# Optimization experiments

Measured on AMD Instinct MI355X. Metric: run time of the kernel, lower is better.

Reference implementation:

```python
import jax, jax.numpy as jnp
import numpy as np

GAMMA = 0.5
BATCH, DIM, UNITS = 16384, 512, 1024


def setup_inputs() -> dict:
    key = jax.random.key(0)
    k1, k2 = jax.random.split(key)
    inputs = jax.random.normal(k1, (BATCH, DIM), dtype=jnp.float32)
    mu = jax.random.normal(k2, (DIM, UNITS), dtype=jnp.float32)
    return {"inputs": inputs, "mu": mu}


def reference(inputs, mu):
    # Squared L2 distance from each input row to each center (column of mu):
    x_sq = jnp.sum(inputs * inputs, axis=1, keepdims=True)        # [B, 1]
    mu_sq = jnp.sum(mu * mu, axis=0, keepdims=True)               # [1, U]
    cross = inputs @ mu                                           # [B, U] GEMM
    l2 = x_sq - 2.0 * cross + mu_sq                                # [B, U]
    return jnp.exp(-GAMMA * l2)
```

## Files before the change

kernel.cpp:

```cpp
#include <hip/hip_runtime.h>
#include <hip/hip_bf16.h>

#define BATCH 16384
#define DIM   512
#define UNITS 1024

typedef float v16f __attribute__((ext_vector_type(16)));

#define APITCH 516
#define BPITCH 33

__global__ __launch_bounds__(256)
void prep_kernel(const float* __restrict__ in, const float* __restrict__ mu,
                 unsigned char* __restrict__ A8f, unsigned char* __restrict__ B8f,
                 float* __restrict__ xsq, float* __restrict__ musq) {
    __shared__ __attribute__((aligned(16))) char smem[512 * BPITCH * 4 + 1024];
    const int t  = threadIdx.x;
    const int l  = t & 63, w = t >> 6;
    const int ln = l & 31, h = l >> 5;

    if (blockIdx.x >= UNITS / 32) {
        float* lds = (float*)smem;
        float* red = (float*)(smem + 32 * APITCH * 4);
        const int c = blockIdx.x - UNITS / 32;
        const float4* src = (const float4*)(in + (size_t)c * 32 * DIM);
        float4* l4 = (float4*)lds;
#pragma unroll
        for (int i = 0; i < 16; i++) {
            const int f = i * 256 + t;
            l4[(f >> 7) * (APITCH / 4) + (f & 127)] = src[f];
        }
        __syncthreads();
        float s = 0.f;
#pragma unroll
        for (int j = 0; j < 8; j++) {
            const int kw = w * 8 + j;
            const float* p = lds + ln * APITCH + kw * 16 + h * 8;
            float4 f0 = *(const float4*)p;
            float4 f1 = *(const float4*)(p + 4);
            s += f0.x * f0.x + f0.y * f0.y + f0.z * f0.z + f0.w * f0.w
               + f1.x * f1.x + f1.y * f1.y + f1.z * f1.z + f1.w * f1.w;
            int lo = __builtin_amdgcn_cvt_pk_fp8_f32(f0.x, f0.y, 0, false);
            lo     = __builtin_amdgcn_cvt_pk_fp8_f32(f0.z, f0.w, lo, true);
            int hi = __builtin_amdgcn_cvt_pk_fp8_f32(f1.x, f1.y, 0, false);
            hi     = __builtin_amdgcn_cvt_pk_fp8_f32(f1.z, f1.w, hi, true);
            *(int2*)(A8f + (((size_t)c * 32 + kw) * 64 + l) * 8) = make_int2(lo, hi);
        }
        red[ln * 8 + w * 2 + h] = s;
        __syncthreads();
        if (t < 32) {
            float a = 0.f;
#pragma unroll
            for (int i = 0; i < 8; i++) a += red[t * 8 + i];
            xsq[c * 32 + t] = a;
        }
    } else {
        float* lds = (float*)smem;
        float* red = (float*)(smem + 512 * BPITCH * 4);
        const int nb = blockIdx.x;
        const int n0 = nb * 32;
        const int col = t & 31, kg = t >> 5;
        float s = 0.f;
        for (int i = 0; i < 64; i++) {
            const int k = i * 8 + kg;
            float v = mu[(size_t)k * UNITS + n0 + col];
            s += v * v;
            lds[k * BPITCH + col] = v;
        }
        red[col * 8 + kg] = s;
        __syncthreads();
        if (t < 32) {
            float a = 0.f;
#pragma unroll
            for (int i = 0; i < 8; i++) a += red[t * 8 + i];
            musq[n0 + t] = a;
        }
#pragma unroll
        for (int j = 0; j < 8; j++) {
            const int kw = w * 8 + j;
            const float* p = lds + (kw * 16 + h * 8) * BPITCH + ln;
            float f[8];
#pragma unroll
            for (int i = 0; i < 8; i++) f[i] = p[i * BPITCH];
            int lo = __builtin_amdgcn_cvt_pk_fp8_f32(f[0], f[1], 0, false);
            lo     = __builtin_amdgcn_cvt_pk_fp8_f32(f[2], f[3], lo, true);
            int hi = __builtin_amdgcn_cvt_pk_fp8_f32(f[4], f[5], 0, false);
            hi     = __builtin_amdgcn_cvt_pk_fp8_f32(f[6], f[7], hi, true);
            *(int2*)(B8f + (((size_t)nb * 32 + kw) * 64 + l) * 8) = make_int2(lo, hi);
        }
    }
}

__global__ __launch_bounds__(256, 4)
void rbf_gemm_kernel(const unsigned char* __restrict__ A8f,
                     const unsigned char* __restrict__ B8f,
                     const float* __restrict__ xsq,
                     const float* __restrict__ musq,
                     float* __restrict__ out) {
    const int t  = threadIdx.x;
    const int l  = t & 63;
    const int w  = t >> 6;
    const int ln = l & 31;
    const int h  = l >> 5;

    const int b  = blockIdx.x;
    const int x  = b & 7;
    const int q  = b >> 3;
    const int rg = q & 15;
    const int cg = q >> 4;
    const int m0 = x * 2048 + rg * 128 + (w >> 1) * 64;
    const int n0 = cg * 128 + (w & 1) * 64;

    const long* Af = (const long*)A8f + (size_t)(m0 >> 5) * 2048 + l;
    const long* Bf = (const long*)B8f + (size_t)(n0 >> 5) * 2048 + l;

    v16f acc[2][2];
#pragma unroll
    for (int c = 0; c < 2; c++)
#pragma unroll
        for (int j = 0; j < 2; j++) acc[c][j] = (v16f)0.f;

#pragma unroll 4
    for (int kw = 0; kw < 32; kw++) {
        long a0 = Af[kw * 64];
        long a1 = Af[2048 + kw * 64];
        long b0 = Bf[kw * 64];
        long b1 = Bf[2048 + kw * 64];
        acc[0][0] = __builtin_amdgcn_mfma_f32_32x32x16_fp8_fp8(a0, b0, acc[0][0], 0, 0, 0);
        acc[0][1] = __builtin_amdgcn_mfma_f32_32x32x16_fp8_fp8(a0, b1, acc[0][1], 0, 0, 0);
        acc[1][0] = __builtin_amdgcn_mfma_f32_32x32x16_fp8_fp8(a1, b0, acc[1][0], 0, 0, 0);
        acc[1][1] = __builtin_amdgcn_mfma_f32_32x32x16_fp8_fp8(a1, b1, acc[1][1], 0, 0, 0);
    }

#pragma unroll
    for (int c = 0; c < 2; c++) {
        const int mc = m0 + c * 32;
        const float xv = -0.5f * xsq[mc + ln];
#pragma unroll
        for (int j = 0; j < 2; j++) {
            const int nc = n0 + j * 32;
            const float mb = -0.5f * musq[nc + ln];
#pragma unroll
            for (int r = 0; r < 16; r++) {
                const int rl = (r & 3) + 8 * (r >> 2) + 4 * h;
                const float xb = __shfl(xv, rl, 64);
                float v = __expf(acc[c][j][r] + xb + mb);
                __builtin_nontemporal_store(
                    v, out + (size_t)(mc + rl) * UNITS + nc + ln);
            }
        }
    }
}

extern "C" void kernel_launch(void* const* d_in, const int* in_sizes, int n_in,
                              void* d_out, int out_size, void* d_ws, size_t ws_size,
                              hipStream_t stream) {
    const float* inputs = (const float*)d_in[0];
    const float* mu     = (const float*)d_in[1];
    float* out = (float*)d_out;

    char* ws = (char*)d_ws;
    unsigned char* A8f = (unsigned char*)ws;
    unsigned char* B8f = (unsigned char*)(ws + (size_t)BATCH * DIM);
    float* xsq  = (float*)(ws + (size_t)BATCH * DIM + (size_t)UNITS * DIM);
    float* musq = xsq + BATCH;

    prep_kernel<<<UNITS / 32 + BATCH / 32, 256, 0, stream>>>(
        inputs, mu, A8f, B8f, xsq, musq);
    rbf_gemm_kernel<<<1024, 256, 0, stream>>>(A8f, B8f, xsq, musq, out);
}
```

Before: 117.6 us.

## Fuse input FP8 quantization and row norms into the GEMM kernel

The prep kernel now only handles mu (FP8 conversion and column norms). Input rows are loaded, squared-summed and converted to FP8 directly inside the GEMM kernel, which stages each 32-row A strip in LDS. Each 512-thread block covers 32 rows by all 1024 units, with each wave computing four 32x32 tiles from a shared A fragment. This removes the write and reread of the FP8 A buffer and the xsq round trip. In exchange, B is reread from global/L2 by every block and the tile shape changes data reuse.

New measurement: 122.9 us. 1.05x slower.

```diff
diff --git a/kernel.cpp b/kernel.cpp
--- a/kernel.cpp
+++ b/kernel.cpp
@@ -7,147 +7,114 @@
 
 typedef float v16f __attribute__((ext_vector_type(16)));
 
-#define APITCH 516
 #define BPITCH 33
+#define FPITCH 520
 
 __global__ __launch_bounds__(256)
-void prep_kernel(const float* __restrict__ in, const float* __restrict__ mu,
-                 unsigned char* __restrict__ A8f, unsigned char* __restrict__ B8f,
-                 float* __restrict__ xsq, float* __restrict__ musq) {
+void prep_b_kernel(const float* __restrict__ mu, unsigned char* __restrict__ B8f,
+                   float* __restrict__ musq) {
     __shared__ __attribute__((aligned(16))) char smem[512 * BPITCH * 4 + 1024];
+    float* lds = (float*)smem;
+    float* red = (float*)(smem + 512 * BPITCH * 4);
     const int t  = threadIdx.x;
     const int l  = t & 63, w = t >> 6;
     const int ln = l & 31, h = l >> 5;
-
-    if (blockIdx.x >= UNITS / 32) {
-        float* lds = (float*)smem;
-        float* red = (float*)(smem + 32 * APITCH * 4);
-        const int c = blockIdx.x - UNITS / 32;
-        const float4* src = (const float4*)(in + (size_t)c * 32 * DIM);
-        float4* l4 = (float4*)lds;
+    const int nb = blockIdx.x;
+    const int n0 = nb * 32;
+    const int col = t & 31, kg = t >> 5;
+    float s = 0.f;
+    for (int i = 0; i < 64; i++) {
+        const int k = i * 8 + kg;
+        float v = mu[(size_t)k * UNITS + n0 + col];
+        s += v * v;
+        lds[k * BPITCH + col] = v;
+    }
+    red[col * 8 + kg] = s;
+    __syncthreads();
+    if (t < 32) {
+        float a = 0.f;
 #pragma unroll
-        for (int i = 0; i < 16; i++) {
-            const int f = i * 256 + t;
-            l4[(f >> 7) * (APITCH / 4) + (f & 127)] = src[f];
-        }
-        __syncthreads();
-        float s = 0.f;
+        for (int i = 0; i < 8; i++) a += red[t * 8 + i];
+        musq[n0 + t] = a;
+    }
 #pragma unroll
-        for (int j = 0; j < 8; j++) {
-            const int kw = w * 8 + j;
-            const float* p = lds + ln * APITCH + kw * 16 + h * 8;
-            float4 f0 = *(const float4*)p;
-            float4 f1 = *(const float4*)(p + 4);
-            s += f0.x * f0.x + f0.y * f0.y + f0.z * f0.z + f0.w * f0.w
-               + f1.x * f1.x + f1.y * f1.y + f1.z * f1.z + f1.w * f1.w;
-            int lo = __builtin_amdgcn_cvt_pk_fp8_f32(f0.x, f0.y, 0, false);
-            lo     = __builtin_amdgcn_cvt_pk_fp8_f32(f0.z, f0.w, lo, true);
-            int hi = __builtin_amdgcn_cvt_pk_fp8_f32(f1.x, f1.y, 0, false);
-            hi     = __builtin_amdgcn_cvt_pk_fp8_f32(f1.z, f1.w, hi, true);
-            *(int2*)(A8f + (((size_t)c * 32 + kw) * 64 + l) * 8) = make_int2(lo, hi);
-        }
-        red[ln * 8 + w * 2 + h] = s;
-        __syncthreads();
-        if (t < 32) {
-            float a = 0.f;
+    for (int j = 0; j < 8; j++) {
+        const int kw = w * 8 + j;
+        const float* p = lds + (kw * 16 + h * 8) * BPITCH + ln;
+        float f[8];
 #pragma unroll
-            for (int i = 0; i < 8; i++) a += red[t * 8 + i];
-            xsq[c * 32 + t] = a;
-        }
-    } else {
-        float* lds = (float*)smem;
-        float* red = (float*)(smem + 512 * BPITCH * 4);
-        const int nb = blockIdx.x;
-        const int n0 = nb * 32;
-        const int col = t & 31, kg = t >> 5;
-        float s = 0.f;
-        for (int i = 0; i < 64; i++) {
-            const int k = i * 8 + kg;
-            float v = mu[(size_t)k * UNITS + n0 + col];
-            s += v * v;
-            lds[k * BPITCH + col] = v;
-        }
-        red[col * 8 + kg] = s;
-        __syncthreads();
-        if (t < 32) {
-            float a = 0.f;
-#pragma unroll
-            for (int i = 0; i < 8; i++) a += red[t * 8 + i];
-            musq[n0 + t] = a;
-        }
-#pragma unroll
-        for (int j = 0; j < 8; j++) {
-            const int kw = w * 8 + j;
-            const float* p = lds + (kw * 16 + h * 8) * BPITCH + ln;
-            float f[8];
-#pragma unroll
-            for (int i = 0; i < 8; i++) f[i] = p[i * BPITCH];
-            int lo = __builtin_amdgcn_cvt_pk_fp8_f32(f[0], f[1], 0, false);
-            lo     = __builtin_amdgcn_cvt_pk_fp8_f32(f[2], f[3], lo, true);
-            int hi = __builtin_amdgcn_cvt_pk_fp8_f32(f[4], f[5], 0, false);
-            hi     = __builtin_amdgcn_cvt_pk_fp8_f32(f[6], f[7], hi, true);
-            *(int2*)(B8f + (((size_t)nb * 32 + kw) * 64 + l) * 8) = make_int2(lo, hi);
-        }
+        for (int i = 0; i < 8; i++) f[i] = p[i * BPITCH];
+        int lo = __builtin_amdgcn_cvt_pk_fp8_f32(f[0], f[1], 0, false);
+        lo     = __builtin_amdgcn_cvt_pk_fp8_f32(f[2], f[3], lo, true);
+        int hi = __builtin_amdgcn_cvt_pk_fp8_f32(f[4], f[5], 0, false);
+        hi     = __builtin_amdgcn_cvt_pk_fp8_f32(f[6], f[7], hi, true);
+        *(int2*)(B8f + (((size_t)nb * 32 + kw) * 64 + l) * 8) = make_int2(lo, hi);
     }
 }
 
-__global__ __launch_bounds__(256, 4)
-void rbf_gemm_kernel(const unsigned char* __restrict__ A8f,
-                     const unsigned char* __restrict__ B8f,
-                     const float* __restrict__ xsq,
-                     const float* __restrict__ musq,
-                     float* __restrict__ out) {
+__global__ __launch_bounds__(512, 4)
+void rbf_fused_kernel(const float* __restrict__ in,
+                      const unsigned char* __restrict__ B8f,
+                      const float* __restrict__ musq,
+                      float* __restrict__ out) {
+    __shared__ __attribute__((aligned(16))) char smem[32 * FPITCH + 256];
+    unsigned char* Af = (unsigned char*)smem;
+    float* red = (float*)(smem + 32 * FPITCH);
+
     const int t  = threadIdx.x;
     const int l  = t & 63;
     const int w  = t >> 6;
     const int ln = l & 31;
     const int h  = l >> 5;
+    const int m0 = blockIdx.x * 32;
 
-    const int b  = blockIdx.x;
-    const int x  = b & 7;
-    const int q  = b >> 3;
-    const int rg = q & 15;
-    const int cg = q >> 4;
-    const int m0 = x * 2048 + rg * 128 + (w >> 1) * 64;
-    const int n0 = cg * 128 + (w & 1) * 64;
+    const float4* src = (const float4*)(in + (size_t)m0 * DIM);
+#pragma unroll
+    for (int i = 0; i < 8; i++) {
+        const int f = i * 512 + t;
+        float4 v = src[f];
+        float ss = v.x * v.x + v.y * v.y + v.z * v.z + v.w * v.w;
+        int p = __builtin_amdgcn_cvt_pk_fp8_f32(v.x, v.y, 0, false);
+        p     = __builtin_amdgcn_cvt_pk_fp8_f32(v.z, v.w, p, true);
+        *(int*)(Af + (f >> 7) * FPITCH + (f & 127) * 4) = p;
+        for (int off = 32; off; off >>= 1) ss += __shfl_down(ss, off, 64);
+        if (l == 0) red[(i * 4 + (w >> 1)) * 2 + (w & 1)] = ss;
+    }
+    __syncthreads();
 
-    const long* Af = (const long*)A8f + (size_t)(m0 >> 5) * 2048 + l;
-    const long* Bf = (const long*)B8f + (size_t)(n0 >> 5) * 2048 + l;
+    const int n0 = w * 128;
+    const long* bptr = (const long*)B8f + (size_t)(n0 >> 5) * 2048 + l;
+    const unsigned char* ap = Af + ln * FPITCH + h * 8;
 
-    v16f acc[2][2];
+    v16f acc[4];
 #pragma unroll
-    for (int c = 0; c < 2; c++)
-#pragma unroll
-        for (int j = 0; j < 2; j++) acc[c][j] = (v16f)0.f;
+    for (int g = 0; g < 4; g++) acc[g] = (v16f)0.f;
 
 #pragma unroll 4
     for (int kw = 0; kw < 32; kw++) {
-        long a0 = Af[kw * 64];
-        long a1 = Af[2048 + kw * 64];
-        long b0 = Bf[kw * 64];
-        long b1 = Bf[2048 + kw * 64];
-        acc[0][0] = __builtin_amdgcn_mfma_f32_32x32x16_fp8_fp8(a0, b0, acc[0][0], 0, 0, 0);
-        acc[0][1] = __builtin_amdgcn_mfma_f32_32x32x16_fp8_fp8(a0, b1, acc[0][1], 0, 0, 0);
-        acc[1][0] = __builtin_amdgcn_mfma_f32_32x32x16_fp8_fp8(a1, b0, acc[1][0], 0, 0, 0);
-        acc[1][1] = __builtin_amdgcn_mfma_f32_32x32x16_fp8_fp8(a1, b1, acc[1][1], 0, 0, 0);
+        long a  = *(const long*)(ap + kw * 16);
+        long b0 = bptr[kw * 64];
+        long b1 = bptr[2048 + kw * 64];
+        long b2 = bptr[4096 + kw * 64];
+        long b3 = bptr[6144 + kw * 64];
+        acc[0] = __builtin_amdgcn_mfma_f32_32x32x16_fp8_fp8(a, b0, acc[0], 0, 0, 0);
+        acc[1] = __builtin_amdgcn_mfma_f32_32x32x16_fp8_fp8(a, b1, acc[1], 0, 0, 0);
+        acc[2] = __builtin_amdgcn_mfma_f32_32x32x16_fp8_fp8(a, b2, acc[2], 0, 0, 0);
+        acc[3] = __builtin_amdgcn_mfma_f32_32x32x16_fp8_fp8(a, b3, acc[3], 0, 0, 0);
     }
 
+    const float xv = -0.5f * (red[ln * 2] + red[ln * 2 + 1]);
 #pragma unroll
-    for (int c = 0; c < 2; c++) {
-        const int mc = m0 + c * 32;
-        const float xv = -0.5f * xsq[mc + ln];
+    for (int g = 0; g < 4; g++) {
+        const int nc = n0 + g * 32;
+        const float mb = -0.5f * musq[nc + ln];
 #pragma unroll
-        for (int j = 0; j < 2; j++) {
-            const int nc = n0 + j * 32;
-            const float mb = -0.5f * musq[nc + ln];
-#pragma unroll
-            for (int r = 0; r < 16; r++) {
-                const int rl = (r & 3) + 8 * (r >> 2) + 4 * h;
-                const float xb = __shfl(xv, rl, 64);
-                float v = __expf(acc[c][j][r] + xb + mb);
-                __builtin_nontemporal_store(
-                    v, out + (size_t)(mc + rl) * UNITS + nc + ln);
-            }
+        for (int r = 0; r < 16; r++) {
+            const int rl = (r & 3) + 8 * (r >> 2) + 4 * h;
+            const float xb = __shfl(xv, rl, 64);
+            float v = __expf(acc[g][r] + xb + mb);
+            __builtin_nontemporal_store(
+                v, out + (size_t)(m0 + rl) * UNITS + nc + ln);
         }
     }
 }
@@ -160,12 +127,9 @@
     float* out = (float*)d_out;
 
     char* ws = (char*)d_ws;
-    unsigned char* A8f = (unsigned char*)ws;
-    unsigned char* B8f = (unsigned char*)(ws + (size_t)BATCH * DIM);
-    float* xsq  = (float*)(ws + (size_t)BATCH * DIM + (size_t)UNITS * DIM);
-    float* musq = xsq + BATCH;
+    unsigned char* B8f = (unsigned char*)ws;
+    float* musq        = (float*)(ws + (size_t)UNITS * DIM);
 
-    prep_kernel<<<UNITS / 32 + BATCH / 32, 256, 0, stream>>>(
-        inputs, mu, A8f, B8f, xsq, musq);
-    rbf_gemm_kernel<<<1024, 256, 0, stream>>>(A8f, B8f, xsq, musq, out);
+    prep_b_kernel<<<UNITS / 32, 256, 0, stream>>>(mu, B8f, musq);
+    rbf_fused_kernel<<<BATCH / 32, 512, 0, stream>>>(inputs, B8f, musq, out);
 }
```

## Stage B tile in LDS via async copy with larger 256x256 blocks

Applied to the files above, without the earlier changes.

The GEMM kernel now uses 1024-thread blocks, each computing a 256x256 output tile. The whole 256-column B slice (128 KB of fp8) is loaded once into LDS with global_load_lds async copies, and all 16 waves share it instead of each wave fetching B from global memory. The prep kernel also remaps its row-block order to interleave across the batch. The 128 KB LDS allocation limits occupancy to one block per CU, and the kernel waits for the full B load before any MFMA work starts.

Result: faster. 112.0 us (-4.7%).

```diff
diff --git a/kernel.cpp b/kernel.cpp
--- a/kernel.cpp
+++ b/kernel.cpp
@@ -9,6 +9,13 @@
 
 #define APITCH 516
 #define BPITCH 33
+
+__device__ __forceinline__ void async_copy16(const void* g, void* l) {
+    __builtin_amdgcn_global_load_lds(
+        (const __attribute__((address_space(1))) void*)g,
+        (__attribute__((address_space(3))) void*)l,
+        16 , 0 , 0 );
+}
 
 __global__ __launch_bounds__(256)
 void prep_kernel(const float* __restrict__ in, const float* __restrict__ mu,
@@ -22,7 +29,8 @@
     if (blockIdx.x >= UNITS / 32) {
         float* lds = (float*)smem;
         float* red = (float*)(smem + 32 * APITCH * 4);
-        const int c = blockIdx.x - UNITS / 32;
+        const int bb = blockIdx.x - UNITS / 32;
+        const int c  = (bb & 7) * 64 + (bb >> 3);
         const float4* src = (const float4*)(in + (size_t)c * 32 * DIM);
         float4* l4 = (float4*)lds;
 #pragma unroll
@@ -91,12 +99,14 @@
     }
 }
 
-__global__ __launch_bounds__(256, 4)
+__global__ __launch_bounds__(1024, 4)
 void rbf_gemm_kernel(const unsigned char* __restrict__ A8f,
                      const unsigned char* __restrict__ B8f,
                      const float* __restrict__ xsq,
                      const float* __restrict__ musq,
                      float* __restrict__ out) {
+    __shared__ __attribute__((aligned(16))) unsigned char Bs[131072];
+
     const int t  = threadIdx.x;
     const int l  = t & 63;
     const int w  = t >> 6;
@@ -105,27 +115,37 @@
 
     const int b  = blockIdx.x;
     const int x  = b & 7;
-    const int q  = b >> 3;
-    const int rg = q & 15;
-    const int cg = q >> 4;
-    const int m0 = x * 2048 + rg * 128 + (w >> 1) * 64;
-    const int n0 = cg * 128 + (w & 1) * 64;
+    const int j  = b >> 3;
+    const int mt = x * 8 + (j & 7);
+    const int nt = j >> 3;
+    const int m0 = mt * 256;
+    const int n0 = nt * 256;
+    const int wm = (w >> 2) * 64;
+    const int wn = (w & 3) * 64;
 
-    const long* Af = (const long*)A8f + (size_t)(m0 >> 5) * 2048 + l;
-    const long* Bf = (const long*)B8f + (size_t)(n0 >> 5) * 2048 + l;
+    const unsigned char* bsrc = B8f + (size_t)n0 * 512;
+#pragma unroll
+    for (int i = 0; i < 8; i++) {
+        const int c = i * 1024 + t;
+        async_copy16(bsrc + c * 16, Bs + c * 16);
+    }
+    __syncthreads();
+
+    const long* Af  = (const long*)A8f + (size_t)((m0 + wm) >> 5) * 2048 + l;
+    const long* lbp = (const long*)Bs + (size_t)(wn >> 5) * 2048 + l;
 
     v16f acc[2][2];
 #pragma unroll
     for (int c = 0; c < 2; c++)
 #pragma unroll
-        for (int j = 0; j < 2; j++) acc[c][j] = (v16f)0.f;
+        for (int g = 0; g < 2; g++) acc[c][g] = (v16f)0.f;
 
 #pragma unroll 4
     for (int kw = 0; kw < 32; kw++) {
         long a0 = Af[kw * 64];
         long a1 = Af[2048 + kw * 64];
-        long b0 = Bf[kw * 64];
-        long b1 = Bf[2048 + kw * 64];
+        long b0 = lbp[kw * 64];
+        long b1 = lbp[2048 + kw * 64];
         acc[0][0] = __builtin_amdgcn_mfma_f32_32x32x16_fp8_fp8(a0, b0, acc[0][0], 0, 0, 0);
         acc[0][1] = __builtin_amdgcn_mfma_f32_32x32x16_fp8_fp8(a0, b1, acc[0][1], 0, 0, 0);
         acc[1][0] = __builtin_amdgcn_mfma_f32_32x32x16_fp8_fp8(a1, b0, acc[1][0], 0, 0, 0);
@@ -134,17 +154,17 @@
 
 #pragma unroll
     for (int c = 0; c < 2; c++) {
-        const int mc = m0 + c * 32;
+        const int mc = m0 + wm + c * 32;
         const float xv = -0.5f * xsq[mc + ln];
 #pragma unroll
-        for (int j = 0; j < 2; j++) {
-            const int nc = n0 + j * 32;
+        for (int g = 0; g < 2; g++) {
+            const int nc = n0 + wn + g * 32;
             const float mb = -0.5f * musq[nc + ln];
 #pragma unroll
             for (int r = 0; r < 16; r++) {
                 const int rl = (r & 3) + 8 * (r >> 2) + 4 * h;
                 const float xb = __shfl(xv, rl, 64);
-                float v = __expf(acc[c][j][r] + xb + mb);
+                float v = __expf(acc[c][g][r] + xb + mb);
                 __builtin_nontemporal_store(
                     v, out + (size_t)(mc + rl) * UNITS + nc + ln);
             }
@@ -167,5 +187,5 @@
 
     prep_kernel<<<UNITS / 32 + BATCH / 32, 256, 0, stream>>>(
         inputs, mu, A8f, B8f, xsq, musq);
-    rbf_gemm_kernel<<<1024, 256, 0, stream>>>(A8f, B8f, xsq, musq, out);
+    rbf_gemm_kernel<<<256, 1024, 0, stream>>>(A8f, B8f, xsq, musq, out);
 }
```
